# Kernel tuning notes

Hardware: AMD Instinct MI355X
Metric: run time of the kernel (lower is better)

The kernel has to match this reference:

```python
import jax, jax.numpy as jnp
import numpy as np

N, D, H, E = 50000, 64, 4, 400000
LN_EPS = 1e-5


def setup_inputs() -> dict:
    key = jax.random.key(0)
    ks = jax.random.split(key, 8)
    x = jax.random.normal(ks[0], (N, D), dtype=jnp.float32)
    edge_index = jax.random.randint(ks[1], (2, E), 0, N, dtype=jnp.int64)
    # nn.Linear(dim, dim*heads, bias=False): weight shape (H*D, D)
    W_lin = jax.random.normal(ks[2], (H * D, D), dtype=jnp.float32) * (1.0 / np.sqrt(D))
    attn_src = jax.random.normal(ks[3], (H, D), dtype=jnp.float32) * 0.1
    attn_dst = jax.random.normal(ks[4], (H, D), dtype=jnp.float32) * 0.1
    # nn.Linear(dim*heads, dim): weight (D, H*D), bias (D,)
    W_out = jax.random.normal(ks[5], (D, H * D), dtype=jnp.float32) * (1.0 / np.sqrt(H * D))
    b_out = jnp.zeros((D,), dtype=jnp.float32)
    ln_g = jnp.ones((D,), dtype=jnp.float32)
    ln_b = jnp.zeros((D,), dtype=jnp.float32)
    return {"x": x, "edge_index": edge_index, "W_lin": W_lin,
            "attn_src": attn_src, "attn_dst": attn_dst,
            "W_out": W_out, "b_out": b_out, "ln_g": ln_g, "ln_b": ln_b}


def reference(x, edge_index, W_lin, attn_src, attn_dst, W_out, b_out, ln_g, ln_b):
    n = x.shape[0]
    i, j = edge_index[0], edge_index[1]  # dst, src node ids per edge
    xh = (x @ W_lin.T).reshape(n, H, D)                 # [N,H,D]
    # per-node attention contributions (equivalent to per-edge dot in source)
    s_dst = jnp.einsum('nhd,hd->nh', xh, attn_dst)      # [N,H]
    s_src = jnp.einsum('nhd,hd->nh', xh, attn_src)      # [N,H]
    alpha = jax.nn.leaky_relu(s_dst[i] + s_src[j], 0.2) # [E,H]
    alpha_exp = jnp.exp(alpha)                          # source uses raw exp (no max-shift)
    denom = jax.ops.segment_sum(alpha_exp, i, num_segments=n)  # [N,H]
    attn = alpha_exp / (denom[i] + 1e-9)                # [E,H]
    msg = attn[:, :, None] * xh[j]                      # [E,H,D]
    out = jax.ops.segment_sum(msg, i, num_segments=n)   # [N,H,D]
    out = out.reshape(n, H * D) @ W_out.T + b_out       # [N,D]
    y = jax.nn.elu(out) + x
    mu = jnp.mean(y, axis=-1, keepdims=True)
    var = jnp.mean(jnp.square(y - mu), axis=-1, keepdims=True)
    return (y - mu) * jax.lax.rsqrt(var + LN_EPS) * ln_g + ln_b
```

## Files before the change

kernel.cpp:

```cpp
#include <hip/hip_runtime.h>

#define N_NODES 50000
#define DIM     64
#define HEADS   4
#define NEDGES  400000
#define HD      256
#define MAXDEG  32
#define NPREP   256
#define ZSTRIDE 264

#define USE_DOT2 1

typedef _Float16 half2v __attribute__((ext_vector_type(2)));
typedef _Float16 half4v __attribute__((ext_vector_type(4)));
typedef _Float16 half8v __attribute__((ext_vector_type(8)));
typedef float    f32x4  __attribute__((ext_vector_type(4)));

union EU { int2 i2; half4v h; };
union HU { unsigned int u; half2v h; };

__device__ __forceinline__ half2v h2cast(unsigned int u) { HU c; c.u = u; return c.h; }

#if USE_DOT2
#define DOT2(a, b, c) __builtin_amdgcn_fdot2((a), (b), (c), false)
#else
__device__ __forceinline__ float DOT2(half2v a, half2v b, float c) {
    return fmaf((float)a[1], (float)b[1], fmaf((float)a[0], (float)b[0], c));
}
#endif

__global__ __launch_bounds__(256) void k_prep(
    const float* __restrict__ x,
    const float* __restrict__ W_lin,
    const float* __restrict__ attn_src,
    const float* __restrict__ attn_dst,
    const float* __restrict__ W_out,
    const int* __restrict__ ei,
    _Float16* __restrict__ G2T,
    _Float16* __restrict__ x16,
    float* __restrict__ S,
    int* __restrict__ cnt,
    int* __restrict__ bucketJ)
{
    __shared__ float weffsh[512];
    const int b = blockIdx.x, t = threadIdx.x;

    for (int e = b * 256 + t; e < NEDGES; e += NPREP * 256) {
        const int i = ei[e];
        const int j = ei[NEDGES + e];
        const int slot = atomicAdd(&cnt[i], 1);
        if (slot < MAXDEG) bucketJ[(size_t)i * MAXDEG + slot] = j;
    }

    for (int id = t; id < 512; id += 256) {
        const int sd = id >> 8, rem = id & 255, h = rem >> 6, k = rem & 63;
        const float* av = sd ? attn_dst : attn_src;
        float acc = 0.f;
        for (int d = 0; d < DIM; ++d)
            acc = fmaf(av[h * DIM + d], W_lin[(h * DIM + d) * DIM + k], acc);
        weffsh[id] = acc;
    }

    {
        const int id = b * 256 + t;
        if (id < 64 * 256) {
            const int d = id >> 8, rem = id & 255, m = rem >> 2, h = rem & 3;
            float acc = 0.f;
            for (int k = 0; k < DIM; ++k)
                acc = fmaf(W_lin[(h * DIM + k) * DIM + m],
                           W_out[d * HD + h * DIM + k], acc);
            G2T[d * HD + m * 4 + h] = (_Float16)acc;
        }
    }
    __syncthreads();

    for (int base = b * 32; base < N_NODES; base += NPREP * 32) {
        const int ni = base + (t >> 3);
        if (ni < N_NODES) {
            const int combo = t & 7;
            const float4* xr = (const float4*)(x + (size_t)ni * DIM);
            const float4* wr = (const float4*)(weffsh + combo * DIM);
            float acc = 0.f;
#pragma unroll
            for (int kp = 0; kp < 16; ++kp) {
                const float4 a = xr[kp], bw = wr[kp];
                acc = fmaf(a.x, bw.x, acc);
                acc = fmaf(a.y, bw.y, acc);
                acc = fmaf(a.z, bw.z, acc);
                acc = fmaf(a.w, bw.w, acc);
            }
            S[(size_t)ni * 8 + combo] = acc;
        }
        const size_t e0 = (size_t)base * DIM + (size_t)t * 8;
        if (e0 + 8 <= (size_t)N_NODES * DIM) {
            const float4 u = *(const float4*)(x + e0);
            const float4 v = *(const float4*)(x + e0 + 4);
            half8v hv;
            hv[0]=(_Float16)u.x; hv[1]=(_Float16)u.y; hv[2]=(_Float16)u.z; hv[3]=(_Float16)u.w;
            hv[4]=(_Float16)v.x; hv[5]=(_Float16)v.y; hv[6]=(_Float16)v.z; hv[7]=(_Float16)v.w;
            *(half8v*)(x16 + e0) = hv;
        }
    }
}

__global__ __launch_bounds__(256) void k_ga(
    const int* __restrict__ cnt,
    const int* __restrict__ bucketJ,
    const float* __restrict__ S,
    const _Float16* __restrict__ x16,
    const _Float16* __restrict__ G2T,
    const float* __restrict__ b_out,
    const float* __restrict__ ln_g,
    const float* __restrict__ ln_b,
    float* __restrict__ out)
{
    __shared__ _Float16 znsh[16 * ZSTRIDE];
    __shared__ float ysh[16][68];
    __shared__ int2  esh[16 * 32];

    const int t = threadIdx.x, wv = t >> 6, l = t & 63;
    const int n0 = blockIdx.x * 16;
    const int side = l >> 5, p = l & 31;

    const int4 degv = *(const int4*)(cnt + n0 + wv * 4);

    int Jr[4];
#pragma unroll
    for (int r = 0; r < 4; ++r)
        Jr[r] = bucketJ[(unsigned)(n0 + wv * 4 + r) * MAXDEG + p];

    float4 SDr[4];
#pragma unroll
    for (int r = 0; r < 4; ++r)
        SDr[r] = *(const float4*)(S + (unsigned)(n0 + wv * 4 + r) * 8 + 4);

    int degc[4];
    degc[0] = degv.x < MAXDEG ? degv.x : MAXDEG;
    degc[1] = degv.y < MAXDEG ? degv.y : MAXDEG;
    degc[2] = degv.z < MAXDEG ? degv.z : MAXDEG;
    degc[3] = degv.w < MAXDEG ? degv.w : MAXDEG;

#pragma unroll
    for (int r = 0; r < 4; ++r)
        Jr[r] = (p < degc[r]) ? Jr[r] : 0;

    float4 SSr[4];
#pragma unroll
    for (int r = 0; r < 4; ++r)
        SSr[r] = *(const float4*)(S + (unsigned)Jr[r] * 8);

#pragma unroll
    for (int r = 0; r < 4; ++r) {
        float u;
        u = SDr[r].x + SSr[r].x; u = u > 0.f ? u : 0.2f * u; const float e0 = __expf(u);
        u = SDr[r].y + SSr[r].y; u = u > 0.f ? u : 0.2f * u; const float e1 = __expf(u);
        u = SDr[r].z + SSr[r].z; u = u > 0.f ? u : 0.2f * u; const float e2 = __expf(u);
        u = SDr[r].w + SSr[r].w; u = u > 0.f ? u : 0.2f * u; const float e3 = __expf(u);
        EU pk;
        pk.h[0] = (_Float16)e0; pk.h[1] = (_Float16)e1;
        pk.h[2] = (_Float16)e2; pk.h[3] = (_Float16)e3;
        int2 ev = pk.i2;
        if (p >= degc[r]) { ev.x = 0; ev.y = 0; }
        if (side == 0) esh[(wv * 4 + r) * 32 + p] = ev;
    }
    __builtin_amdgcn_wave_barrier();

    struct Grp { half2v xv[4]; int2 ee[4]; };
    float za[4], zb[4], dd[4];
    const half2v one2 = h2cast(0x3C003C00u);

    auto stage_group = [&](int r, int s, Grp& g) {
        const int jb = s + side;
#pragma unroll
        for (int q = 0; q < 4; ++q) {
            const int jv = __shfl(Jr[r], jb + 2 * q, 64);
            g.xv[q] = *(const half2v*)(x16 + (unsigned)jv * DIM + (p << 1));
        }
        const int eb = (wv * 4 + r) * 32 + jb;
#pragma unroll
        for (int q = 0; q < 4; ++q)
            g.ee[q] = esh[eb + 2 * q];
    };

    auto consume_group = [&](const Grp& g) {
#pragma unroll
        for (int pp = 0; pp < 2; ++pp) {
            const int2 ea = g.ee[2 * pp], eb2 = g.ee[2 * pp + 1];
            HU xa, xb; xa.h = g.xv[2 * pp]; xb.h = g.xv[2 * pp + 1];
            const unsigned E0 = __builtin_amdgcn_perm(eb2.x, ea.x, 0x05040100u);
            const unsigned E1 = __builtin_amdgcn_perm(eb2.x, ea.x, 0x07060302u);
            const unsigned E2 = __builtin_amdgcn_perm(eb2.y, ea.y, 0x05040100u);
            const unsigned E3 = __builtin_amdgcn_perm(eb2.y, ea.y, 0x07060302u);
            const unsigned XA = __builtin_amdgcn_perm(xb.u, xa.u, 0x05040100u);
            const unsigned XB = __builtin_amdgcn_perm(xb.u, xa.u, 0x07060302u);
            const half2v f0 = h2cast(E0), f1 = h2cast(E1);
            const half2v f2 = h2cast(E2), f3 = h2cast(E3);
            const half2v va = h2cast(XA), vb = h2cast(XB);
            za[0] = DOT2(f0, va, za[0]); za[1] = DOT2(f1, va, za[1]);
            za[2] = DOT2(f2, va, za[2]); za[3] = DOT2(f3, va, za[3]);
            zb[0] = DOT2(f0, vb, zb[0]); zb[1] = DOT2(f1, vb, zb[1]);
            zb[2] = DOT2(f2, vb, zb[2]); zb[3] = DOT2(f3, vb, zb[3]);
            dd[0] = DOT2(f0, one2, dd[0]); dd[1] = DOT2(f1, one2, dd[1]);
            dd[2] = DOT2(f2, one2, dd[2]); dd[3] = DOT2(f3, one2, dd[3]);
        }
    };

    Grp cur, nxt, remb;
    stage_group(0, 0, cur);

#pragma unroll
    for (int r = 0; r < 4; ++r) {
        const bool rem = degc[r] > 8;
        if (rem) stage_group(r, 8, remb);
        if (r < 3) stage_group(r + 1, 0, nxt);

#pragma unroll
        for (int h = 0; h < 4; ++h) { za[h] = 0.f; zb[h] = 0.f; dd[h] = 0.f; }

        consume_group(cur);
        if (rem) {
            consume_group(remb);
            for (int s = 16; s < degc[r]; s += 8) {
                Grp tg;
                stage_group(r, s, tg);
                consume_group(tg);
            }
        }

#pragma unroll
        for (int h = 0; h < 4; ++h) {
            dd[h] += __shfl_xor(dd[h], 32, 64);
            za[h] += __shfl_xor(za[h], 32, 64);
            zb[h] += __shfl_xor(zb[h], 32, 64);
        }
        const float r0 = __builtin_amdgcn_rcpf(dd[0] + 1e-9f);
        const float r1 = __builtin_amdgcn_rcpf(dd[1] + 1e-9f);
        const float r2 = __builtin_amdgcn_rcpf(dd[2] + 1e-9f);
        const float r3 = __builtin_amdgcn_rcpf(dd[3] + 1e-9f);
        if (side == 0) {
            half8v o;
            o[0] = (_Float16)(za[0] * r0); o[1] = (_Float16)(za[1] * r1);
            o[2] = (_Float16)(za[2] * r2); o[3] = (_Float16)(za[3] * r3);
            o[4] = (_Float16)(zb[0] * r0); o[5] = (_Float16)(zb[1] * r1);
            o[6] = (_Float16)(zb[2] * r2); o[7] = (_Float16)(zb[3] * r3);
            *(half8v*)(znsh + (wv * 4 + r) * ZSTRIDE + p * 8) = o;
        }
        cur = nxt;
    }
    __syncthreads();

    const int mrow = l & 15, quad = l >> 4;
    half8v A[8];
    const _Float16* zr = znsh + mrow * ZSTRIDE + quad * 8;
#pragma unroll
    for (int s = 0; s < 8; ++s)
        A[s] = *(const half8v*)(zr + 32 * s);

    const _Float16* gp = G2T + (size_t)(wv * 16 + mrow) * HD + quad * 8;
    f32x4 c0 = {0.f, 0.f, 0.f, 0.f}, c1 = {0.f, 0.f, 0.f, 0.f};
#pragma unroll
    for (int s = 0; s < 4; ++s)
        c0 = __builtin_amdgcn_mfma_f32_16x16x32_f16(A[s], *(const half8v*)(gp + 32 * s), c0, 0, 0, 0);
#pragma unroll
    for (int s = 4; s < 8; ++s)
        c1 = __builtin_amdgcn_mfma_f32_16x16x32_f16(A[s], *(const half8v*)(gp + 32 * s), c1, 0, 0, 0);
    const f32x4 c = c0 + c1;

    const int col = wv * 16 + mrow;
    const float bo = b_out[col];
#pragma unroll
    for (int rho = 0; rho < 4; ++rho) {
        const int nl = quad * 4 + rho;
        const float o = c[rho] + bo;
        const float eo = o > 0.f ? o : expm1f(o);
        ysh[nl][col] = eo + (float)x16[(size_t)(n0 + nl) * DIM + col];
    }
    __syncthreads();

    {
        const int g = l >> 4, c4 = (l & 15) * 4;
        const int nl = wv * 4 + g;
        const float4 yv = *(const float4*)(&ysh[nl][c4]);
        float s1 = (yv.x + yv.y) + (yv.z + yv.w);
        float s2 = fmaf(yv.x, yv.x, fmaf(yv.y, yv.y, fmaf(yv.z, yv.z, yv.w * yv.w)));
#pragma unroll
        for (int off = 8; off > 0; off >>= 1) {
            s1 += __shfl_xor(s1, off, 64);
            s2 += __shfl_xor(s2, off, 64);
        }
        const float mu = s1 * (1.f / 64.f);
        const float var = fmaf(-mu, mu, s2 * (1.f / 64.f));
        const float rr = rsqrtf(var + 1e-5f);
        const float4 gv = *(const float4*)(ln_g + c4);
        const float4 bv = *(const float4*)(ln_b + c4);
        float4 ov;
        ov.x = (yv.x - mu) * rr * gv.x + bv.x;
        ov.y = (yv.y - mu) * rr * gv.y + bv.y;
        ov.z = (yv.z - mu) * rr * gv.z + bv.z;
        ov.w = (yv.w - mu) * rr * gv.w + bv.w;
        *(float4*)(out + (size_t)(n0 + nl) * DIM + c4) = ov;
    }
}

extern "C" void kernel_launch(void* const* d_in, const int* in_sizes, int n_in,
                              void* d_out, int out_size, void* d_ws, size_t ws_size,
                              hipStream_t stream)
{
    const float* x        = (const float*)d_in[0];
    const int*   ei       = (const int*)d_in[1];
    const float* W_lin    = (const float*)d_in[2];
    const float* attn_src = (const float*)d_in[3];
    const float* attn_dst = (const float*)d_in[4];
    const float* W_out    = (const float*)d_in[5];
    const float* b_out    = (const float*)d_in[6];
    const float* ln_g     = (const float*)d_in[7];
    const float* ln_b     = (const float*)d_in[8];
    float* out = (float*)d_out;

    char* ws = (char*)d_ws;
    _Float16* x16    = (_Float16*)ws;
    float*    S      = (float*)(x16 + (size_t)N_NODES * DIM);
    _Float16* G2T    = (_Float16*)(S + (size_t)N_NODES * 8);
    int*      cnt    = (int*)(G2T + 64 * HD);
    int*      bucketJ= cnt + N_NODES;

    hipMemsetAsync(cnt, 0, (size_t)N_NODES * sizeof(int), stream);

    k_prep<<<NPREP, 256, 0, stream>>>(x, W_lin, attn_src, attn_dst, W_out, ei,
                                      G2T, x16, S, cnt, bucketJ);

    k_ga<<<N_NODES / 16, 256, 0, stream>>>(cnt, bucketJ, S, x16, G2T,
                                           b_out, ln_g, ln_b, out);
}
```

Baseline: 147.2 us.

## Widen prep grid to one node tile per block, hoist x loads, split accumulators

Raises the prep kernel's grid from 256 to 2048 blocks, so each block handles exactly one 32-node tile and the node loop disappears. The x loads for the fp16 conversion are issued at kernel start, before the edge bucketing, so their latency overlaps the atomics. The small weight-folding and score dot products now use four independent accumulators to shorten FMA dependency chains, and the shared weight array is padded. The cost is that every block redundantly recomputes the 512-entry folded attention weights from W_lin, eight times as often as before.

```diff
diff --git a/kernel.cpp b/kernel.cpp
--- a/kernel.cpp
+++ b/kernel.cpp
@@ -6,7 +6,7 @@
 #define NEDGES  400000
 #define HD      256
 #define MAXDEG  32
-#define NPREP   256
+#define NPREP   2048
 #define ZSTRIDE 264
 
 #define USE_DOT2 1
@@ -42,8 +42,17 @@
     int* __restrict__ cnt,
     int* __restrict__ bucketJ)
 {
-    __shared__ float weffsh[512];
+    __shared__ float weffsh[8][68];
     const int b = blockIdx.x, t = threadIdx.x;
+    const int base = b * 32;
+
+    const size_t e0 = (size_t)base * DIM + (size_t)t * 8;
+    const bool do_x = (e0 + 8 <= (size_t)N_NODES * DIM);
+    float4 u = {0.f, 0.f, 0.f, 0.f}, v = {0.f, 0.f, 0.f, 0.f};
+    if (do_x) {
+        u = *(const float4*)(x + e0);
+        v = *(const float4*)(x + e0 + 4);
+    }
 
     for (int e = b * 256 + t; e < NEDGES; e += NPREP * 256) {
         const int i = ei[e];
@@ -55,46 +64,59 @@
     for (int id = t; id < 512; id += 256) {
         const int sd = id >> 8, rem = id & 255, h = rem >> 6, k = rem & 63;
         const float* av = sd ? attn_dst : attn_src;
-        float acc = 0.f;
-        for (int d = 0; d < DIM; ++d)
-            acc = fmaf(av[h * DIM + d], W_lin[(h * DIM + d) * DIM + k], acc);
-        weffsh[id] = acc;
+        float a0 = 0.f, a1 = 0.f, a2 = 0.f, a3 = 0.f;
+#pragma unroll
+        for (int d = 0; d < DIM; d += 4) {
+            a0 = fmaf(av[h * DIM + d],     W_lin[(h * DIM + d)     * DIM + k], a0);
+            a1 = fmaf(av[h * DIM + d + 1], W_lin[(h * DIM + d + 1) * DIM + k], a1);
+            a2 = fmaf(av[h * DIM + d + 2], W_lin[(h * DIM + d + 2) * DIM + k], a2);
+            a3 = fmaf(av[h * DIM + d + 3], W_lin[(h * DIM + d + 3) * DIM + k], a3);
+        }
+        weffsh[sd * 4 + h][k] = (a0 + a1) + (a2 + a3);
     }
 
     {
         const int id = b * 256 + t;
         if (id < 64 * 256) {
             const int d = id >> 8, rem = id & 255, m = rem >> 2, h = rem & 3;
-            float acc = 0.f;
-            for (int k = 0; k < DIM; ++k)
-                acc = fmaf(W_lin[(h * DIM + k) * DIM + m],
-                           W_out[d * HD + h * DIM + k], acc);
-            G2T[d * HD + m * 4 + h] = (_Float16)acc;
+            float a0 = 0.f, a1 = 0.f, a2 = 0.f, a3 = 0.f;
+#pragma unroll
+            for (int k = 0; k < DIM; k += 4) {
+                a0 = fmaf(W_lin[(h * DIM + k)     * DIM + m], W_out[d * HD + h * DIM + k],     a0);
+                a1 = fmaf(W_lin[(h * DIM + k + 1) * DIM + m], W_out[d * HD + h * DIM + k + 1], a1);
+                a2 = fmaf(W_lin[(h * DIM + k + 2) * DIM + m], W_out[d * HD + h * DIM + k + 2], a2);
+                a3 = fmaf(W_lin[(h * DIM + k + 3) * DIM + m], W_out[d * HD + h * DIM + k + 3], a3);
+            }
+            G2T[d * HD + m * 4 + h] = (_Float16)((a0 + a1) + (a2 + a3));
         }
     }
     __syncthreads();
 
-    for (int base = b * 32; base < N_NODES; base += NPREP * 32) {
+    {
         const int ni = base + (t >> 3);
         if (ni < N_NODES) {
             const int combo = t & 7;
             const float4* xr = (const float4*)(x + (size_t)ni * DIM);
-            const float4* wr = (const float4*)(weffsh + combo * DIM);
-            float acc = 0.f;
-#pragma unroll
-            for (int kp = 0; kp < 16; ++kp) {
-                const float4 a = xr[kp], bw = wr[kp];
-                acc = fmaf(a.x, bw.x, acc);
-                acc = fmaf(a.y, bw.y, acc);
-                acc = fmaf(a.z, bw.z, acc);
-                acc = fmaf(a.w, bw.w, acc);
+            const float4* wr = (const float4*)(weffsh[combo]);
+            float a0 = 0.f, a1 = 0.f, a2 = 0.f, a3 = 0.f;
+#pragma unroll
+            for (int kp = 0; kp < 16; kp += 4) {
+                const float4 xa = xr[kp],     wa = wr[kp];
+                const float4 xb = xr[kp + 1], wb = wr[kp + 1];
+                const float4 xc = xr[kp + 2], wc = wr[kp + 2];
+                const float4 xd = xr[kp + 3], wd = wr[kp + 3];
+                a0 = fmaf(xa.x, wa.x, a0); a0 = fmaf(xa.y, wa.y, a0);
+                a0 = fmaf(xa.z, wa.z, a0); a0 = fmaf(xa.w, wa.w, a0);
+                a1 = fmaf(xb.x, wb.x, a1); a1 = fmaf(xb.y, wb.y, a1);
+                a1 = fmaf(xb.z, wb.z, a1); a1 = fmaf(xb.w, wb.w, a1);
+                a2 = fmaf(xc.x, wc.x, a2); a2 = fmaf(xc.y, wc.y, a2);
+                a2 = fmaf(xc.z, wc.z, a2); a2 = fmaf(xc.w, wc.w, a2);
+                a3 = fmaf(xd.x, wd.x, a3); a3 = fmaf(xd.y, wd.y, a3);
+                a3 = fmaf(xd.z, wd.z, a3); a3 = fmaf(xd.w, wd.w, a3);
             }
-            S[(size_t)ni * 8 + combo] = acc;
-        }
-        const size_t e0 = (size_t)base * DIM + (size_t)t * 8;
-        if (e0 + 8 <= (size_t)N_NODES * DIM) {
-            const float4 u = *(const float4*)(x + e0);
-            const float4 v = *(const float4*)(x + e0 + 4);
+            S[(size_t)ni * 8 + combo] = (a0 + a1) + (a2 + a3);
+        }
+        if (do_x) {
             half8v hv;
             hv[0]=(_Float16)u.x; hv[1]=(_Float16)u.y; hv[2]=(_Float16)u.z; hv[3]=(_Float16)u.w;
             hv[4]=(_Float16)v.x; hv[5]=(_Float16)v.y; hv[6]=(_Float16)v.z; hv[7]=(_Float16)v.w;
```

Result: no change. 146.6 us (-0.4%).
